# Performance work log

Measured on AMD Instinct MI355X. Metric: run time of the kernel, lower is better.

Reference implementation:

```python
import jax, jax.numpy as jnp
import numpy as np

B, T, C = 4, 1024, 1024  # batch, tokens, channel (== head `size`)
H = 8                    # num_heads


def setup_inputs() -> dict:
    key = jax.random.key(0)
    kd, kq, kk, kv = jax.random.split(key, 4)
    data = jax.random.normal(kd, (B, T, C), dtype=jnp.float32)
    # torch nn.Linear(size,size,bias=False) weight is [out,in]; one per head, stacked on axis 0
    s = 1.0 / np.sqrt(C)
    Wq = jax.random.uniform(kq, (H, C, C), dtype=jnp.float32, minval=-s, maxval=s)
    Wk = jax.random.uniform(kk, (H, C, C), dtype=jnp.float32, minval=-s, maxval=s)
    Wv = jax.random.uniform(kv, (H, C, C), dtype=jnp.float32, minval=-s, maxval=s)
    return {"data": data, "Wq": Wq, "Wk": Wk, "Wv": Wv}


def reference(data, Wq, Wk, Wv):
    # per-head projections: y = x @ W.T  -> [B,H,T,C]
    q = jnp.einsum('btc,hdc->bhtd', data, Wq)
    k = jnp.einsum('btc,hdc->bhtd', data, Wk)
    v = jnp.einsum('btc,hdc->bhtd', data, Wv)
    scale = 1.0 / jnp.sqrt(jnp.asarray(C, dtype=data.dtype))
    scores = jnp.einsum('bhtd,bhsd->bhts', q, k) * scale  # [B,H,T,T]
    causal = jnp.tril(jnp.ones((T, T), dtype=bool))
    scores = jnp.where(causal, scores, -jnp.inf)
    w = jax.nn.softmax(scores, axis=-1)
    out = jnp.einsum('bhts,bhsd->bhtd', w, v)            # [B,H,T,C]
    # torch.cat over heads on last dim == [B,T,H,C] reshape to [B,T,H*C]
    return out.transpose(0, 2, 1, 3).reshape(B, T, H * C)
```

## Files before the change

kernel.cpp:

```cpp
#include <hip/hip_runtime.h>
#include <hip/hip_fp16.h>


typedef unsigned short u16;
typedef _Float16 f16x8 __attribute__((ext_vector_type(8)));
typedef float f32x4 __attribute__((ext_vector_type(4)));

__device__ __forceinline__ u16 f2h(float f) {
    union { __half h; u16 u; } cv;
    cv.h = __float2half(f);
    return cv.u;
}
__device__ __forceinline__ float h2f(u16 u) {
    union { __half h; u16 u; } cv;
    cv.u = u;
    return __half2float(cv.h);
}

__device__ __forceinline__ void gload_lds16(const u16* g, const u16* lds_base, unsigned off_bytes) {
    unsigned a32 = (unsigned)(uintptr_t)((const char*)lds_base + off_bytes);
    a32 = __builtin_amdgcn_readfirstlane(a32);
    __builtin_amdgcn_global_load_lds(
        (const __attribute__((address_space(1))) void*)(uintptr_t)g,
        (__attribute__((address_space(3))) void*)a32,
        16, 0, 0);
}

#define M_PROJ 0
#define M_QK 1
#define M_PV 2

template <int MODE>
__global__ __launch_bounds__(512, 2) void mega(
    const u16* __restrict__ dataH, const u16* __restrict__ WqH,
    const u16* __restrict__ WkH, const u16* __restrict__ WvH,
    u16* __restrict__ Qa, u16* __restrict__ Ka, u16* __restrict__ VTa,
    u16* __restrict__ S16, const u16* __restrict__ P16,
    float* __restrict__ outF)
{
    const int C = 1024, T = 1024, HC = 8192;
    const int nb = (MODE == M_PROJ ? 1536 : MODE == M_QK ? 320 : 512);
    const int chunk = nb >> 3;
    const int phys = blockIdx.x;
    const int o = (phys & 7) * chunk + (phys >> 3);

    const u16 *Ab, *Bb;
    int lda, ldb, ldc, NT, tile_m, tile_n;
    float scale = 1.0f;
    u16* out16 = nullptr;
    float* out32 = nullptr;

    if (MODE == M_PROJ) {
        const int g = o >> 9, r = o & 511;
        if (g < 2) {
            const int s = r >> 6, ww = r & 63;
            tile_n = (s & 3) * 8 + (ww & 7);
            tile_m = (s >> 2) * 8 + (ww >> 3);
            Ab = dataH + (size_t)tile_m * 256 * C;
            Bb = (g ? WkH : WqH) + (size_t)tile_n * 256 * C;
            lda = C; ldb = C; ldc = HC;
            out16 = g ? Ka : Qa;
            NT = 16;
        } else {
            const int vz = r >> 4, rem = r & 15;
            tile_n = rem & 3; tile_m = rem >> 2;
            Ab = WvH + (size_t)(vz & 7) * C * C + (size_t)tile_m * 256 * C;
            Bb = dataH + (size_t)(vz >> 3) * T * C + (size_t)tile_n * 256 * C;
            lda = C; ldb = C; ldc = T;
            out16 = VTa + (size_t)vz * C * T;
            NT = 16;
        }
    } else if (MODE == M_QK) {
        const int qz = o / 10, j = o - qz * 10;
        tile_m = (j >= 1) + (j >= 3) + (j >= 6);
        tile_n = j - (tile_m == 0 ? 0 : tile_m == 1 ? 1 : tile_m == 2 ? 3 : 6);
        const size_t zo = (size_t)(qz >> 3) * T * HC + (size_t)(qz & 7) * C;
        Ab = Qa + zo + (size_t)tile_m * 256 * HC;
        Bb = Ka + zo + (size_t)tile_n * 256 * HC;
        lda = HC; ldb = HC; ldc = T;
        out16 = S16 + (size_t)qz * T * T;
        scale = 1.0f / 32.0f;
        NT = 16;
    } else {
        const int x = o & 3, y = (o >> 2) & 3, pz = o >> 4;
        tile_m = 3 - y;
        tile_n = x;
        Ab = P16 + (size_t)pz * T * T + (size_t)tile_m * 256 * T;
        Bb = VTa + (size_t)pz * C * T + (size_t)tile_n * 256 * T;
        lda = T; ldb = T; ldc = HC;
        out32 = outF + (size_t)(pz >> 3) * T * HC + (size_t)(pz & 7) * C;
        NT = (tile_m + 1) * 4;
    }

    __shared__ u16 lds[8 * 8192];

    const int t = threadIdx.x, w = t >> 6, l = t & 63;
    const int wm = w >> 2, wn = w & 3;
    const int frow = l & 15, fch = l >> 4;

    const int clin = w * 64 + l;
    const int srow = clin >> 2;
    const int sch = (clin & 3) ^ ((clin >> 3) & 3);
    const long eA = (long)srow * lda + sch * 8;
    const long eB = (long)srow * ldb + sch * 8;

    f32x4 acc[8][4] = {};
    f16x8 af[4], bf[4];

#define STAGE(DB, MAT, KS, TT) do {                                            \
        const u16* g_ = (MAT == 0 ? Ab + (size_t)(TT) * 64 + (KS) * 32 + eA    \
                                  : Bb + (size_t)(TT) * 64 + (KS) * 32 + eB);  \
        const u16* hb_ = lds + ((((DB) << 2) | ((MAT) << 1) | (KS)) << 13);    \
        gload_lds16(g_, hb_, (unsigned)(w * 64 * 16));                         \
        gload_lds16(g_ + (size_t)128 * (MAT == 0 ? lda : ldb), hb_,            \
                    (unsigned)((512 + w * 64) * 16));                          \
    } while (0)

#define RD(DB, MAT, KS, ROW)                                                   \
    (*(const f16x8*)((const char*)(lds + ((((DB) << 2) | ((MAT) << 1) | (KS)) << 13)) + \
                     ((unsigned)((ROW) * 64 + fch * 16) ^ ((((ROW) >> 1) & 3) << 4))))

#define VM6 do { asm volatile("s_waitcnt vmcnt(6)"); \
                 __builtin_amdgcn_sched_barrier(0); } while (0)
#define VM0 do { asm volatile("s_waitcnt vmcnt(0)"); \
                 __builtin_amdgcn_sched_barrier(0); } while (0)
#define NOPW ((void)0)

#define PH(DB, KS, MH, WAITC, ...) do {                                        \
        if ((MH) == 0) {                                                       \
            _Pragma("unroll") for (int ni = 0; ni < 4; ++ni)                   \
                bf[ni] = RD(DB, 1, KS, wn * 64 + ni * 16 + frow);              \
        }                                                                      \
        _Pragma("unroll") for (int m4 = 0; m4 < 4; ++m4)                       \
            af[m4] = RD(DB, 0, KS, wm * 128 + ((MH) * 4 + m4) * 16 + frow);    \
        __VA_ARGS__;                                                           \
        __builtin_amdgcn_sched_barrier(0);                                     \
        __builtin_amdgcn_s_barrier();                                          \
        asm volatile("s_waitcnt lgkmcnt(0)");                                  \
        __builtin_amdgcn_sched_barrier(0);                                     \
        __builtin_amdgcn_s_setprio(1);                                         \
        _Pragma("unroll") for (int m4 = 0; m4 < 4; ++m4)                       \
            _Pragma("unroll") for (int ni = 0; ni < 4; ++ni)                   \
                acc[(MH) * 4 + m4][ni] = __builtin_amdgcn_mfma_f32_16x16x32_f16( \
                    af[m4], bf[ni], acc[(MH) * 4 + m4][ni], 0, 0, 0);          \
        __builtin_amdgcn_s_setprio(0);                                         \
        __builtin_amdgcn_sched_barrier(0);                                     \
        WAITC;                                                                 \
        __builtin_amdgcn_s_barrier();                                          \
    } while (0)

    STAGE(0, 1, 0, 0); STAGE(0, 0, 0, 0); STAGE(0, 1, 1, 0); STAGE(0, 0, 1, 0);
    STAGE(1, 1, 0, 1); STAGE(1, 0, 0, 1); STAGE(1, 1, 1, 1);
    VM6;
    __builtin_amdgcn_s_barrier();

    for (int tt = 0; tt < NT; tt += 2) {
        const bool more = (tt + 2) < NT;
        PH(0, 0, 0, NOPW, STAGE(1, 0, 1, tt + 1));
        PH(0, 0, 1, NOPW, if (more) STAGE(0, 1, 0, tt + 2));
        PH(0, 1, 0, NOPW, if (more) STAGE(0, 0, 0, tt + 2));
        PH(0, 1, 1, if (more) VM6; else VM0,
                    if (more) STAGE(0, 1, 1, tt + 2));
        PH(1, 0, 0, NOPW, if (more) STAGE(0, 0, 1, tt + 2));
        PH(1, 0, 1, NOPW, if (more) STAGE(1, 1, 0, tt + 3));
        PH(1, 1, 0, NOPW, if (more) STAGE(1, 0, 0, tt + 3));
        PH(1, 1, 1, if (more) VM6; else VM0,
                    if (more) STAGE(1, 1, 1, tt + 3));
    }
#undef PH
#undef RD
#undef STAGE

    const int r0 = (l >> 4) * 4, cc = l & 15;
#pragma unroll
    for (int mi = 0; mi < 8; ++mi) {
#pragma unroll
        for (int r = 0; r < 4; ++r) {
            size_t grow = (size_t)(tile_m * 256 + wm * 128 + mi * 16 + r0 + r);
#pragma unroll
            for (int ni = 0; ni < 4; ++ni) {
                int gcol = tile_n * 256 + wn * 64 + ni * 16 + cc;
                float v = acc[mi][ni][r] * scale;
                if (MODE == M_PV)
                    out32[grow * ldc + gcol] = v;
                else
                    out16[grow * ldc + gcol] = f2h(v);
            }
        }
    }
}

__global__ __launch_bounds__(256) void softmax16(
    const u16* __restrict__ S, u16* __restrict__ P)
{
    const int T = 1024;
    const int tq = blockIdx.x, z = blockIdx.y;
    const u16* row = S + ((size_t)z * T + tq) * T;
    u16* prow = P + ((size_t)z * T + tq) * T;
    const int n = tq + 1, tid = threadIdx.x, i0 = tid * 4;
    const int nw = ((tq >> 8) + 1) << 8;

    ushort4 v = ((const ushort4*)row)[tid];
    float e0 = (i0 + 0 < n) ? h2f(v.x) : -1e30f;
    float e1 = (i0 + 1 < n) ? h2f(v.y) : -1e30f;
    float e2 = (i0 + 2 < n) ? h2f(v.z) : -1e30f;
    float e3 = (i0 + 3 < n) ? h2f(v.w) : -1e30f;

    float m = fmaxf(fmaxf(e0, e1), fmaxf(e2, e3));
#pragma unroll
    for (int o = 1; o < 64; o <<= 1) m = fmaxf(m, __shfl_xor(m, o));
    __shared__ float red[4];
    if ((tid & 63) == 0) red[tid >> 6] = m;
    __syncthreads();
    m = fmaxf(fmaxf(red[0], red[1]), fmaxf(red[2], red[3]));

    float p0 = __expf(e0 - m), p1 = __expf(e1 - m);
    float p2 = __expf(e2 - m), p3 = __expf(e3 - m);
    float s = p0 + p1 + p2 + p3;
#pragma unroll
    for (int o = 1; o < 64; o <<= 1) s += __shfl_xor(s, o);
    __shared__ float red2[4];
    if ((tid & 63) == 0) red2[tid >> 6] = s;
    __syncthreads();
    const float inv = 1.0f / (red2[0] + red2[1] + red2[2] + red2[3]);

    if (i0 < nw) {
        ushort4 o4;
        o4.x = f2h(p0 * inv); o4.y = f2h(p1 * inv);
        o4.z = f2h(p2 * inv); o4.w = f2h(p3 * inv);
        ((ushort4*)prow)[tid] = o4;
    }
}

__global__ __launch_bounds__(256) void cast_all(
    const float* __restrict__ d0, const float* __restrict__ w1,
    const float* __restrict__ w2, const float* __restrict__ w3,
    u16* __restrict__ dst)
{
    const int n0 = 1048576, nW = 2097152;
    for (int i = blockIdx.x * 256 + threadIdx.x; i < 7340032; i += 524288) {
        float4 v;
        if (i < n0)               v = ((const float4*)d0)[i];
        else if (i < n0 + nW)     v = ((const float4*)w1)[i - n0];
        else if (i < n0 + 2 * nW) v = ((const float4*)w2)[i - n0 - nW];
        else                      v = ((const float4*)w3)[i - n0 - 2 * nW];
        ushort4 o4;
        o4.x = f2h(v.x); o4.y = f2h(v.y); o4.z = f2h(v.z); o4.w = f2h(v.w);
        ((ushort4*)dst)[i] = o4;
    }
}

extern "C" void kernel_launch(void* const* d_in, const int* in_sizes, int n_in,
                              void* d_out, int out_size, void* d_ws, size_t ws_size,
                              hipStream_t stream)
{
    (void)in_sizes; (void)n_in; (void)out_size; (void)ws_size;
    const int B = 4, T = 1024, C = 1024, H = 8;
    const int BT = B * T, HC = H * C;

    const float* data = (const float*)d_in[0];
    const float* Wq = (const float*)d_in[1];
    const float* Wk = (const float*)d_in[2];
    const float* Wv = (const float*)d_in[3];
    float* out = (float*)d_out;

    char* p = (char*)d_ws;
    const size_t nData = (size_t)BT * C;
    const size_t nW = (size_t)H * C * C;
    const size_t nAll = (size_t)BT * HC;
    const size_t nS = (size_t)B * H * T * T;
    u16* dataH = (u16*)p; p += nData * 2;
    u16* WqH = (u16*)p; p += nW * 2;
    u16* WkH = (u16*)p; p += nW * 2;
    u16* WvH = (u16*)p; p += nW * 2;
    u16* Qa = (u16*)p; p += nAll * 2;
    u16* Ka = (u16*)p; p += nAll * 2;
    u16* VTa = (u16*)p; p += nAll * 2;
    u16* S16 = (u16*)p; p += nS * 2;
    u16* P16 = (u16*)p; p += nS * 2;

    cast_all<<<dim3(2048), dim3(256), 0, stream>>>(data, Wq, Wk, Wv, dataH);

    mega<M_PROJ><<<dim3(1536), dim3(512), 0, stream>>>(
        dataH, WqH, WkH, WvH, Qa, Ka, VTa, S16, P16, out);

    mega<M_QK><<<dim3(320), dim3(512), 0, stream>>>(
        dataH, WqH, WkH, WvH, Qa, Ka, VTa, S16, P16, out);

    softmax16<<<dim3(T, B * H), dim3(256), 0, stream>>>(S16, P16);

    mega<M_PV><<<dim3(512), dim3(512), 0, stream>>>(
        dataH, WqH, WkH, WvH, Qa, Ka, VTa, S16, P16, out);
}
```

Before: 433.9 us.

## Fold Wq^T Wk into per-head matrix and drop K projection

Scores are rewritten as x·(Wq^T Wk)·x^T. A new GEMM stage builds a per-head C×C matrix M from transposed Wq and Wk, then projects data through M once and multiplies that against raw data in the QK stage, so the K projection and its buffer go away. The cast kernel now transposes Wq and Wk through shared memory. The PV stage pairs causal row tiles (3 with 0, 2 with 1) in a two-pass block to balance work across half as many blocks. This removes one B·T·C·H projection GEMM in exchange for an extra H·C³ GEMM and an extra kernel launch, and changes fp16 rounding of the intermediate products.

New measurement: 384.8 us. 1.13x faster.

```diff
diff --git a/kernel.cpp b/kernel.cpp
--- a/kernel.cpp
+++ b/kernel.cpp
@@ -26,86 +26,99 @@
         16, 0, 0);
 }
 
-#define M_PROJ 0
-#define M_QK 1
-#define M_PV 2
+#define M_MT 0
+#define M_PROJ 1
+#define M_QK 2
+#define M_PV 3
 
 template <int MODE>
 __global__ __launch_bounds__(512, 2) void mega(
-    const u16* __restrict__ dataH, const u16* __restrict__ WqH,
-    const u16* __restrict__ WkH, const u16* __restrict__ WvH,
-    u16* __restrict__ Qa, u16* __restrict__ Ka, u16* __restrict__ VTa,
+    const u16* __restrict__ dataH, const u16* __restrict__ WvH,
+    const u16* __restrict__ WqT, const u16* __restrict__ WkT,
+    u16* __restrict__ MTp, u16* __restrict__ Qp, u16* __restrict__ VTa,
     u16* __restrict__ S16, const u16* __restrict__ P16,
     float* __restrict__ outF)
 {
     const int C = 1024, T = 1024, HC = 8192;
-    const int nb = (MODE == M_PROJ ? 1536 : MODE == M_QK ? 320 : 512);
+    const int nb = (MODE == M_MT ? 128 : MODE == M_PROJ ? 1024 :
+                    MODE == M_QK ? 320 : 256);
     const int chunk = nb >> 3;
     const int phys = blockIdx.x;
     const int o = (phys & 7) * chunk + (phys >> 3);
 
-    const u16 *Ab, *Bb;
-    int lda, ldb, ldc, NT, tile_m, tile_n;
-    float scale = 1.0f;
-    u16* out16 = nullptr;
-    float* out32 = nullptr;
-
-    if (MODE == M_PROJ) {
-        const int g = o >> 9, r = o & 511;
-        if (g < 2) {
-            const int s = r >> 6, ww = r & 63;
-            tile_n = (s & 3) * 8 + (ww & 7);
-            tile_m = (s >> 2) * 8 + (ww >> 3);
-            Ab = dataH + (size_t)tile_m * 256 * C;
-            Bb = (g ? WkH : WqH) + (size_t)tile_n * 256 * C;
-            lda = C; ldb = C; ldc = HC;
-            out16 = g ? Ka : Qa;
-            NT = 16;
-        } else {
-            const int vz = r >> 4, rem = r & 15;
-            tile_n = rem & 3; tile_m = rem >> 2;
-            Ab = WvH + (size_t)(vz & 7) * C * C + (size_t)tile_m * 256 * C;
-            Bb = dataH + (size_t)(vz >> 3) * T * C + (size_t)tile_n * 256 * C;
-            lda = C; ldb = C; ldc = T;
-            out16 = VTa + (size_t)vz * C * T;
-            NT = 16;
-        }
-    } else if (MODE == M_QK) {
-        const int qz = o / 10, j = o - qz * 10;
-        tile_m = (j >= 1) + (j >= 3) + (j >= 6);
-        tile_n = j - (tile_m == 0 ? 0 : tile_m == 1 ? 1 : tile_m == 2 ? 3 : 6);
-        const size_t zo = (size_t)(qz >> 3) * T * HC + (size_t)(qz & 7) * C;
-        Ab = Qa + zo + (size_t)tile_m * 256 * HC;
-        Bb = Ka + zo + (size_t)tile_n * 256 * HC;
-        lda = HC; ldb = HC; ldc = T;
-        out16 = S16 + (size_t)qz * T * T;
-        scale = 1.0f / 32.0f;
-        NT = 16;
-    } else {
-        const int x = o & 3, y = (o >> 2) & 3, pz = o >> 4;
-        tile_m = 3 - y;
-        tile_n = x;
-        Ab = P16 + (size_t)pz * T * T + (size_t)tile_m * 256 * T;
-        Bb = VTa + (size_t)pz * C * T + (size_t)tile_n * 256 * T;
-        lda = T; ldb = T; ldc = HC;
-        out32 = outF + (size_t)(pz >> 3) * T * HC + (size_t)(pz & 7) * C;
-        NT = (tile_m + 1) * 4;
-    }
-
     __shared__ u16 lds[8 * 8192];
 
     const int t = threadIdx.x, w = t >> 6, l = t & 63;
     const int wm = w >> 2, wn = w & 3;
     const int frow = l & 15, fch = l >> 4;
-
     const int clin = w * 64 + l;
     const int srow = clin >> 2;
     const int sch = (clin & 3) ^ ((clin >> 3) & 3);
-    const long eA = (long)srow * lda + sch * 8;
-    const long eB = (long)srow * ldb + sch * 8;
-
-    f32x4 acc[8][4] = {};
-    f16x8 af[4], bf[4];
+
+    const int NPASS = (MODE == M_PV) ? 2 : 1;
+
+    for (int pass = 0; pass < NPASS; ++pass) {
+        const u16 *Ab, *Bb;
+        int lda, ldb, ldc, NT, tile_m, tile_n;
+        float scale = 1.0f;
+        u16* out16 = nullptr;
+        float* out32 = nullptr;
+
+        if (MODE == M_MT) {
+            const int h = o >> 4, r = o & 15;
+            tile_m = r >> 2; tile_n = r & 3;
+            Ab = WkT + (size_t)h * C * C + (size_t)tile_m * 256 * C;
+            Bb = WqT + (size_t)h * C * C + (size_t)tile_n * 256 * C;
+            lda = C; ldb = C; ldc = C;
+            out16 = MTp + (size_t)h * C * C;
+            NT = 16;
+        } else if (MODE == M_PROJ) {
+            const int g = o >> 9, r = o & 511;
+            if (g == 0) {
+                const int s = r >> 6, ww = r & 63;
+                tile_n = (s & 3) * 8 + (ww & 7);
+                tile_m = (s >> 2) * 8 + (ww >> 3);
+                Ab = dataH + (size_t)tile_m * 256 * C;
+                Bb = MTp + (size_t)(tile_n >> 2) * C * C + (size_t)(tile_n & 3) * 256 * C;
+                lda = C; ldb = C; ldc = HC;
+                out16 = Qp;
+                NT = 16;
+            } else {
+                const int vz = r >> 4, rem = r & 15;
+                tile_n = rem & 3; tile_m = rem >> 2;
+                Ab = WvH + (size_t)(vz & 7) * C * C + (size_t)tile_m * 256 * C;
+                Bb = dataH + (size_t)(vz >> 3) * T * C + (size_t)tile_n * 256 * C;
+                lda = C; ldb = C; ldc = T;
+                out16 = VTa + (size_t)vz * C * T;
+                NT = 16;
+            }
+        } else if (MODE == M_QK) {
+            const int qz = o / 10, j = o - qz * 10;
+            tile_m = (j >= 1) + (j >= 3) + (j >= 6);
+            tile_n = j - (tile_m == 0 ? 0 : tile_m == 1 ? 1 : tile_m == 2 ? 3 : 6);
+            Ab = Qp + (size_t)(qz >> 3) * T * HC + (size_t)(qz & 7) * C
+                    + (size_t)tile_m * 256 * HC;
+            Bb = dataH + (size_t)(qz >> 3) * T * C + (size_t)tile_n * 256 * C;
+            lda = HC; ldb = C; ldc = T;
+            out16 = S16 + (size_t)qz * T * T;
+            scale = 1.0f / 32.0f;
+            NT = 16;
+        } else {
+            const int pz = o >> 3, j = o & 7, x = j & 3, hi = j >> 2;
+            tile_m = (pass == 0) ? (hi ? 2 : 3) : (hi ? 1 : 0);
+            tile_n = x;
+            Ab = P16 + (size_t)pz * T * T + (size_t)tile_m * 256 * T;
+            Bb = VTa + (size_t)pz * C * T + (size_t)tile_n * 256 * T;
+            lda = T; ldb = T; ldc = HC;
+            out32 = outF + (size_t)(pz >> 3) * T * HC + (size_t)(pz & 7) * C;
+            NT = (tile_m + 1) * 4;
+        }
+
+        const long eA = (long)srow * lda + sch * 8;
+        const long eB = (long)srow * ldb + sch * 8;
+
+        f32x4 acc[8][4] = {};
+        f16x8 af[4], bf[4];
 
 #define STAGE(DB, MAT, KS, TT) do {                                            \
         const u16* g_ = (MAT == 0 ? Ab + (size_t)(TT) * 64 + (KS) * 32 + eA    \
@@ -149,42 +162,46 @@
         __builtin_amdgcn_s_barrier();                                          \
     } while (0)
 
-    STAGE(0, 1, 0, 0); STAGE(0, 0, 0, 0); STAGE(0, 1, 1, 0); STAGE(0, 0, 1, 0);
-    STAGE(1, 1, 0, 1); STAGE(1, 0, 0, 1); STAGE(1, 1, 1, 1);
-    VM6;
-    __builtin_amdgcn_s_barrier();
-
-    for (int tt = 0; tt < NT; tt += 2) {
-        const bool more = (tt + 2) < NT;
-        PH(0, 0, 0, NOPW, STAGE(1, 0, 1, tt + 1));
-        PH(0, 0, 1, NOPW, if (more) STAGE(0, 1, 0, tt + 2));
-        PH(0, 1, 0, NOPW, if (more) STAGE(0, 0, 0, tt + 2));
-        PH(0, 1, 1, if (more) VM6; else VM0,
-                    if (more) STAGE(0, 1, 1, tt + 2));
-        PH(1, 0, 0, NOPW, if (more) STAGE(0, 0, 1, tt + 2));
-        PH(1, 0, 1, NOPW, if (more) STAGE(1, 1, 0, tt + 3));
-        PH(1, 1, 0, NOPW, if (more) STAGE(1, 0, 0, tt + 3));
-        PH(1, 1, 1, if (more) VM6; else VM0,
-                    if (more) STAGE(1, 1, 1, tt + 3));
-    }
+        STAGE(0, 1, 0, 0); STAGE(0, 0, 0, 0); STAGE(0, 1, 1, 0); STAGE(0, 0, 1, 0);
+        STAGE(1, 1, 0, 1); STAGE(1, 0, 0, 1); STAGE(1, 1, 1, 1);
+        VM6;
+        __builtin_amdgcn_s_barrier();
+
+        for (int tt = 0; tt < NT; tt += 2) {
+            const bool more = (tt + 2) < NT;
+            PH(0, 0, 0, NOPW, STAGE(1, 0, 1, tt + 1));
+            PH(0, 0, 1, NOPW, if (more) STAGE(0, 1, 0, tt + 2));
+            PH(0, 1, 0, NOPW, if (more) STAGE(0, 0, 0, tt + 2));
+            PH(0, 1, 1, if (more) VM6; else VM0,
+                        if (more) STAGE(0, 1, 1, tt + 2));
+            PH(1, 0, 0, NOPW, if (more) STAGE(0, 0, 1, tt + 2));
+            PH(1, 0, 1, NOPW, if (more) STAGE(1, 1, 0, tt + 3));
+            PH(1, 1, 0, NOPW, if (more) STAGE(1, 0, 0, tt + 3));
+            PH(1, 1, 1, if (more) VM6; else VM0,
+                        if (more) STAGE(1, 1, 1, tt + 3));
+        }
 #undef PH
 #undef RD
 #undef STAGE
-
-    const int r0 = (l >> 4) * 4, cc = l & 15;
-#pragma unroll
-    for (int mi = 0; mi < 8; ++mi) {
-#pragma unroll
-        for (int r = 0; r < 4; ++r) {
-            size_t grow = (size_t)(tile_m * 256 + wm * 128 + mi * 16 + r0 + r);
-#pragma unroll
-            for (int ni = 0; ni < 4; ++ni) {
-                int gcol = tile_n * 256 + wn * 64 + ni * 16 + cc;
-                float v = acc[mi][ni][r] * scale;
-                if (MODE == M_PV)
-                    out32[grow * ldc + gcol] = v;
-                else
-                    out16[grow * ldc + gcol] = f2h(v);
+#undef VM6
+#undef VM0
+#undef NOPW
+
+        const int r0 = (l >> 4) * 4, cc = l & 15;
+#pragma unroll
+        for (int mi = 0; mi < 8; ++mi) {
+#pragma unroll
+            for (int r = 0; r < 4; ++r) {
+                size_t grow = (size_t)(tile_m * 256 + wm * 128 + mi * 16 + r0 + r);
+#pragma unroll
+                for (int ni = 0; ni < 4; ++ni) {
+                    int gcol = tile_n * 256 + wn * 64 + ni * 16 + cc;
+                    float v = acc[mi][ni][r] * scale;
+                    if (MODE == M_PV)
+                        out32[grow * ldc + gcol] = v;
+                    else
+                        out16[grow * ldc + gcol] = f2h(v);
+                }
             }
         }
     }
@@ -232,21 +249,37 @@
     }
 }
 
-__global__ __launch_bounds__(256) void cast_all(
-    const float* __restrict__ d0, const float* __restrict__ w1,
-    const float* __restrict__ w2, const float* __restrict__ w3,
-    u16* __restrict__ dst)
+__global__ __launch_bounds__(256) void cast_setup(
+    const float* __restrict__ data, const float* __restrict__ Wq,
+    const float* __restrict__ Wk, const float* __restrict__ Wv,
+    u16* __restrict__ dataH, u16* __restrict__ WqT,
+    u16* __restrict__ WkT, u16* __restrict__ WvH)
 {
-    const int n0 = 1048576, nW = 2097152;
-    for (int i = blockIdx.x * 256 + threadIdx.x; i < 7340032; i += 524288) {
-        float4 v;
-        if (i < n0)               v = ((const float4*)d0)[i];
-        else if (i < n0 + nW)     v = ((const float4*)w1)[i - n0];
-        else if (i < n0 + 2 * nW) v = ((const float4*)w2)[i - n0 - nW];
-        else                      v = ((const float4*)w3)[i - n0 - 2 * nW];
-        ushort4 o4;
-        o4.x = f2h(v.x); o4.y = f2h(v.y); o4.z = f2h(v.z); o4.w = f2h(v.w);
-        ((ushort4*)dst)[i] = o4;
+    const int z = blockIdx.z, tx = threadIdx.x, ty = threadIdx.y;
+    if (z < 16) {
+        const int h = z & 7;
+        const float* src = ((z >> 3) ? Wk : Wq) + (size_t)h * 1048576;
+        u16* dst = ((z >> 3) ? WkT : WqT) + (size_t)h * 1048576;
+        const int r0 = blockIdx.y * 32, c0 = blockIdx.x * 32;
+        __shared__ float tile[32][33];
+        for (int i = ty; i < 32; i += 8)
+            tile[i][tx] = src[(size_t)(r0 + i) * 1024 + c0 + tx];
+        __syncthreads();
+        for (int i = ty; i < 32; i += 8)
+            dst[(size_t)(c0 + i) * 1024 + r0 + tx] = f2h(tile[tx][i]);
+    } else {
+        const int tid = ty * 32 + tx;
+        const int bid = blockIdx.y * 32 + blockIdx.x;
+        const int reps = (z == 16) ? 4 : 8;
+        const float* src = (z == 16) ? data : Wv;
+        u16* dst = (z == 16) ? dataH : WvH;
+        for (int k2 = 0; k2 < reps; ++k2) {
+            int i = (k2 * 1024 + bid) * 256 + tid;
+            float4 v = ((const float4*)src)[i];
+            ushort4 o4;
+            o4.x = f2h(v.x); o4.y = f2h(v.y); o4.z = f2h(v.z); o4.w = f2h(v.w);
+            ((ushort4*)dst)[i] = o4;
+        }
     }
 }
 
@@ -270,25 +303,29 @@
     const size_t nAll = (size_t)BT * HC;
     const size_t nS = (size_t)B * H * T * T;
     u16* dataH = (u16*)p; p += nData * 2;
-    u16* WqH = (u16*)p; p += nW * 2;
-    u16* WkH = (u16*)p; p += nW * 2;
     u16* WvH = (u16*)p; p += nW * 2;
-    u16* Qa = (u16*)p; p += nAll * 2;
-    u16* Ka = (u16*)p; p += nAll * 2;
+    u16* WqT = (u16*)p; p += nW * 2;
+    u16* WkT = (u16*)p; p += nW * 2;
+    u16* MTp = (u16*)p; p += nW * 2;
+    u16* Qp = (u16*)p; p += nAll * 2;
     u16* VTa = (u16*)p; p += nAll * 2;
     u16* S16 = (u16*)p; p += nS * 2;
     u16* P16 = (u16*)p; p += nS * 2;
 
-    cast_all<<<dim3(2048), dim3(256), 0, stream>>>(data, Wq, Wk, Wv, dataH);
-
-    mega<M_PROJ><<<dim3(1536), dim3(512), 0, stream>>>(
-        dataH, WqH, WkH, WvH, Qa, Ka, VTa, S16, P16, out);
+    cast_setup<<<dim3(32, 32, 18), dim3(32, 8), 0, stream>>>(
+        data, Wq, Wk, Wv, dataH, WqT, WkT, WvH);
+
+    mega<M_MT><<<dim3(128), dim3(512), 0, stream>>>(
+        dataH, WvH, WqT, WkT, MTp, Qp, VTa, S16, P16, out);
+
+    mega<M_PROJ><<<dim3(1024), dim3(512), 0, stream>>>(
+        dataH, WvH, WqT, WkT, MTp, Qp, VTa, S16, P16, out);
 
     mega<M_QK><<<dim3(320), dim3(512), 0, stream>>>(
-        dataH, WqH, WkH, WvH, Qa, Ka, VTa, S16, P16, out);
+        dataH, WvH, WqT, WkT, MTp, Qp, VTa, S16, P16, out);
 
     softmax16<<<dim3(T, B * H), dim3(256), 0, stream>>>(S16, P16);
 
-    mega<M_PV><<<dim3(512), dim3(512), 0, stream>>>(
-        dataH, WqH, WkH, WvH, Qa, Ka, VTa, S16, P16, out);
-}
+    mega<M_PV><<<dim3(256), dim3(512), 0, stream>>>(
+        dataH, WvH, WqT, WkT, MTp, Qp, VTa, S16, P16, out);
+}
```
